# Kernel optimization log

Hardware: AMD Instinct MI355X
Metric: run time of the kernel (lower is better)

The kernel has to match this reference:

```python
import jax, jax.numpy as jnp
import numpy as np


def setup_inputs() -> dict:
    key = jax.random.key(0)
    k1, k2, k3, k4 = jax.random.split(key, 4)
    B, Tv, Ta, D = 8, 2048, 2048, 256
    return {
        "visual_features": jax.random.normal(k1, (B, Tv, D), dtype=jnp.float32),
        "audio_features": jax.random.normal(k2, (B, Ta, D), dtype=jnp.float32),
        "visual_weights": jax.random.uniform(k3, (D, D), dtype=jnp.float32),
        "audio_weights": jax.random.uniform(k4, (D, D), dtype=jnp.float32),
        "num_neighbors": 8,
    }


def _pairwise_l2(vm, am):
    # ||v - a|| via the expanded form to avoid the [B,Tv,Ta,D] intermediate.
    sq = (
        jnp.sum(vm * vm, -1)[:, :, None]
        + jnp.sum(am * am, -1)[:, None, :]
        - 2.0 * jnp.einsum("btd,bsd->bts", vm, am)
    )
    sq = jnp.maximum(sq, 0.0)
    # safe sqrt: subgradient 0 at 0 (matches torch.norm backward convention)
    return jnp.where(sq > 0, jnp.sqrt(jnp.where(sq > 0, sq, 1.0)), 0.0)


def reference(visual_features, audio_features, visual_weights, audio_weights, num_neighbors):
    vm = visual_features @ visual_weights  # [B,Tv,D]
    am = audio_features @ audio_weights    # [B,Ta,D]
    graph = jnp.exp(-_pairwise_l2(vm, am))  # [B,Tv,Ta]
    # topk over the visual axis (dim=1): move it last for lax.top_k
    _, idx = jax.lax.top_k(jnp.swapaxes(graph, 1, 2), num_neighbors)  # [B,Ta,k]
    idx = jnp.swapaxes(idx, 1, 2)  # [B,k,Ta]
    # broadcasted gather along axis 1: result [B,k,Ta,D]
    vn = jnp.take_along_axis(visual_features[:, :, None, :], idx[..., None], axis=1)
    an = jnp.take_along_axis(audio_features[:, :, None, :], idx[..., None], axis=1)
    # mean over dim=2 (the Ta axis of the gathered neighbors) -> [B,k,D]
    return vn.mean(axis=2), an.mean(axis=2)
```

## Files before the change

kernel.cpp:

```cpp
#include <hip/hip_runtime.h>
#include <cstddef>
#include <cstdint>

namespace {
constexpr int kB   = 8;
constexpr int kT   = 2048;
constexpr int kD   = 256;
constexpr int kK   = 8;
constexpr int kM   = kB * kT;
constexpr int kNC  = kB * kT;
constexpr int kColCap = 64;
constexpr int kOvCap  = 1 << 17;
constexpr int kStr = 264;
constexpr float kMinNormalF = 1.17549435e-38f;
}

typedef __attribute__((ext_vector_type(8)))  __bf16 bf16x8;
typedef __attribute__((ext_vector_type(16))) float  f32x16;

__device__ inline unsigned short f2bf_rne(float x) {
  unsigned u = __float_as_uint(x);
  unsigned r = (u + 0x7FFFu + ((u >> 16) & 1u)) >> 16;
  return (unsigned short)r;
}
__device__ inline float bf2f(unsigned short h) {
  return __uint_as_float((unsigned)h << 16);
}
union FragU { uint4 u4; bf16x8 v; };

__device__ inline void async16(const unsigned short* g, unsigned short* l) {
  __builtin_amdgcn_global_load_lds(
      (const __attribute__((address_space(1))) unsigned int*)(const void*)g,
      (__attribute__((address_space(3))) unsigned int*)(void*)l, 16, 0, 0);
}

__device__ inline void stage_tile_async(const unsigned short* src,
                                        unsigned short* S, int w, int lane) {
  const int hi = lane >> 5, lo = lane & 31;
#pragma unroll
  for (int i = 0; i < 8; ++i) {
    const int p = w * 8 + i;
    const int rowl = p * 2 + hi;
    const int c = lo ^ (rowl & 31);
    async16(src + (size_t)rowl * kD + c * 8, S + p * 512);
  }
}
__device__ inline uint4 lds_frag(const unsigned short* S, int row, int kc, int half) {
  const int c = (kc * 2 + half) ^ (row & 31);
  return *reinterpret_cast<const uint4*>(S + row * 256 + c * 8);
}

__global__ __launch_bounds__(256) void prep(const float* __restrict__ W0,
                                            const float* __restrict__ W1,
                                            unsigned short* __restrict__ T0,
                                            unsigned short* __restrict__ T1,
                                            unsigned* __restrict__ zeroBase,
                                            int zeroWords,
                                            unsigned* __restrict__ outW) {
  const int blk = blockIdx.x;
  if (blk < 128) {
    const float* W = (blk & 64) ? W1 : W0;
    unsigned short* WT = (blk & 64) ? T1 : T0;
    const int t = blk & 63;
    const int c0 = (t & 7) * 32, k0 = (t >> 3) * 32;
    __shared__ float tile[32][33];
    const int tx = threadIdx.x & 31, ty = threadIdx.x >> 5;
#pragma unroll
    for (int i = 0; i < 4; ++i)
      tile[ty + i * 8][tx] = W[(size_t)(k0 + ty + i * 8) * kD + c0 + tx];
    __syncthreads();
#pragma unroll
    for (int i = 0; i < 4; ++i)
      WT[(size_t)(c0 + ty + i * 8) * kD + k0 + tx] = f2bf_rne(tile[tx][ty + i * 8]);
  } else {
    for (int i = (blk - 128) * 256 + threadIdx.x; i < zeroWords; i += 32 * 256)
      zeroBase[i] = 0u;
    for (int i = (blk - 128) * 256 + threadIdx.x; i < 2 * kB * kK * kD; i += 32 * 256)
      outW[i] = 0u;
  }
}

__global__ __launch_bounds__(256) void gemm_hyb(const float* __restrict__ Xv,
                                                const float* __restrict__ Xa,
                                                const unsigned short* __restrict__ WvT,
                                                const unsigned short* __restrict__ WaT,
                                                unsigned short* __restrict__ Cv,
                                                unsigned short* __restrict__ Ca,
                                                float* __restrict__ nv,
                                                float* __restrict__ na) {
  __shared__ unsigned short S[64 * kStr + 64 * 256];
  unsigned short* bufA = S;
  unsigned short* bufB = S + 64 * kStr;
  const int z = blockIdx.z;
  const float* X = z ? Xa : Xv;
  const unsigned short* WT = z ? WaT : WvT;
  unsigned short* Cb = z ? Ca : Cv;
  float* nrm = z ? na : nv;
  const int r0 = blockIdx.x * 64;
  const int tid = threadIdx.x;
  const int w = tid >> 6, lane = tid & 63;
  const int wt = w & 1, wc = w >> 1;
  const int half = lane >> 5, ln = lane & 31;

#pragma unroll
  for (int i = 0; i < 16; ++i) {
    const int idx = i * 256 + tid;
    const int row = idx >> 6, g = idx & 63;
    const float4 v = *reinterpret_cast<const float4*>(X + (size_t)(r0 + row) * kD + g * 4);
    ushort4 o;
    o.x = f2bf_rne(v.x); o.y = f2bf_rne(v.y); o.z = f2bf_rne(v.z); o.w = f2bf_rne(v.w);
    *reinterpret_cast<ushort4*>(bufA + row * kStr + g * 4) = o;
  }
  __syncthreads();

  stage_tile_async(WT, bufB, w, lane);
  uint4 afr[16];
#pragma unroll
  for (int kc = 0; kc < 16; ++kc)
    afr[kc] = *reinterpret_cast<const uint4*>(bufA + (wt * 32 + ln) * kStr + kc * 16 + half * 8);
  __syncthreads();

  float ns[16];
#pragma unroll
  for (int r = 0; r < 16; ++r) ns[r] = 0.0f;

  for (int ct = 0; ct < 4; ++ct) {
    unsigned short* cur = (ct & 1) ? bufA : bufB;
    unsigned short* nxt = (ct & 1) ? bufB : bufA;
    if (ct < 3)
      stage_tile_async(WT + (size_t)(ct + 1) * 64 * kD, nxt, w, lane);
    const int c0 = ct * 64;
    f32x16 acc;
#pragma unroll
    for (int i = 0; i < 16; ++i) acc[i] = 0.0f;
#pragma unroll
    for (int kc = 0; kc < 16; ++kc) {
      FragU fa, fb;
      fa.u4 = afr[kc];
      fb.u4 = lds_frag(cur, wc * 32 + ln, kc, half);
      acc = __builtin_amdgcn_mfma_f32_32x32x16_bf16(fa.v, fb.v, acc, 0, 0, 0);
    }
    const int col = c0 + wc * 32 + ln;
#pragma unroll
    for (int r = 0; r < 16; ++r) {
      const int row = r0 + wt * 32 + (r & 3) + 8 * (r >> 2) + 4 * half;
      const unsigned short us = f2bf_rne(acc[r]);
      Cb[(size_t)row * kD + col] = us;
      const float f = bf2f(us);
      ns[r] += f * f;
    }
    if (ct < 3) __syncthreads();
  }
#pragma unroll
  for (int r = 0; r < 16; ++r) {
    float v = ns[r];
#pragma unroll
    for (int off = 1; off < 32; off <<= 1) v += __shfl_xor(v, off, 64);
    if (ln == 0) {
      const int row = r0 + wt * 32 + (r & 3) + 8 * (r >> 2) + 4 * half;
      atomicAdd(nrm + row, v);
    }
  }
}

__global__ __launch_bounds__(256, 4) void keys_v16(const unsigned short* __restrict__ vmb,
                                                   const unsigned short* __restrict__ amb,
                                                   const float* __restrict__ vn2,
                                                   const float* __restrict__ an2,
                                                   unsigned* __restrict__ colCount,
                                                   uint2* __restrict__ colRecs,
                                                   unsigned* __restrict__ ovCount,
                                                   uint2* __restrict__ ovRecs) {
  __shared__ unsigned short S[64 * 256];
  const int hw = blockIdx.x + (blockIdx.y << 4) + (blockIdx.z << 7);
  const int lg = ((hw & 7) << 7) | (hw >> 3);
  const int b = lg >> 7;
  const int t0 = (lg & 15) << 7;
  const int sr0 = ((lg >> 4) & 7) << 8;
  const int tid = threadIdx.x;
  const int w = tid >> 6, lane = tid & 63;
  const int half = lane >> 5, ln = lane & 31;

  uint4 afr[16];
#pragma unroll
  for (int h = 0; h < 2; ++h) {
    __syncthreads();
    stage_tile_async(vmb + ((size_t)b * kT + t0 + h * 64) * kD, S, w, lane);
    __syncthreads();
    if ((w >> 1) == h) {
#pragma unroll
      for (int kc = 0; kc < 16; ++kc)
        afr[kc] = lds_frag(S, (w & 1) * 32 + ln, kc, half);
    }
  }

  const float* v2p = vn2 + (size_t)b * kT + t0 + w * 32;

  for (int st = 0; st < 4; ++st) {
    const int s0 = sr0 + st * 64;
    __syncthreads();
    stage_tile_async(amb + ((size_t)b * kT + s0) * kD, S, w, lane);
    __syncthreads();
#pragma unroll
    for (int ss = 0; ss < 2; ++ss) {
      f32x16 acc;
#pragma unroll
      for (int i = 0; i < 16; ++i) acc[i] = 0.0f;
#pragma unroll
      for (int kc = 0; kc < 16; ++kc) {
        FragU fa, fb;
        fa.u4 = afr[kc];
        fb.u4 = lds_frag(S, ss * 32 + ln, kc, half);
        acc = __builtin_amdgcn_mfma_f32_32x32x16_bf16(fa.v, fb.v, acc, 0, 0, 0);
      }
      const int s = s0 + ss * 32 + ln;
      const float a2 = an2[(size_t)b * kT + s];
      const int c = (b << 11) | s;
#pragma unroll
      for (int g = 0; g < 4; ++g) {
        const float4 v2 = *reinterpret_cast<const float4*>(v2p + g * 8 + half * 4);
        const float v2a[4] = {v2.x, v2.y, v2.z, v2.w};
#pragma unroll
        for (int q = 0; q < 4; ++q) {
          const float raw = v2a[q] + a2 - 2.0f * acc[4 * g + q];
          if (raw < 7744.0f) {
            const float dist = sqrtf(fmaxf(raw, 0.0f));
            const float e = expf(-dist);
            if (e >= kMinNormalF) {
              const int t = t0 + w * 32 + g * 8 + half * 4 + q;
              const unsigned slot = atomicAdd(&colCount[c], 1u);
              if (slot < (unsigned)kColCap) {
                colRecs[(size_t)c * kColCap + slot] = make_uint2(__float_as_uint(e), (unsigned)t);
              } else {
                const unsigned pos = ((unsigned)b << 22) | ((unsigned)s << 11) | (unsigned)t;
                const unsigned oi = atomicAdd(ovCount, 1u);
                if (oi < (unsigned)kOvCap) ovRecs[oi] = make_uint2(__float_as_uint(e), pos);
              }
            }
          }
        }
      }
    }
  }
}

__global__ __launch_bounds__(256) void gather_fused(const float* __restrict__ visual,
                                                    const float* __restrict__ audio,
                                                    const unsigned* __restrict__ colCount,
                                                    const uint2* __restrict__ colRecs,
                                                    const unsigned* __restrict__ ovCount,
                                                    const uint2* __restrict__ ovRecs,
                                                    float* __restrict__ out) {
  __shared__ int sIdx[32];
  const int u = blockIdx.x;
  const int bj = u >> 6, ch = u & 63;
  const int b = bj >> 3, j = bj & 7;
  const int tid = threadIdx.x;
  if (tid < 32) {
    const int s = ch * 32 + tid;
    const int c = (b << 11) | s;
    unsigned K[8]; int T[8];
#pragma unroll
    for (int i = 0; i < 8; ++i) { K[i] = 0u; T[i] = 0x7FFFFFFF; }
    const int cnt = (int)colCount[c];
    const int m = min(cnt, kColCap);
    for (int i = 0; i < m; ++i) {
      const uint2 r = colRecs[(size_t)c * kColCap + i];
      const unsigned kx = r.x; const int tx = (int)r.y;
      if (kx > K[7] || (kx == K[7] && tx < T[7])) {
        K[7] = kx; T[7] = tx;
#pragma unroll
        for (int q = 7; q >= 1; --q) {
          const bool sw = (K[q] > K[q - 1]) || (K[q] == K[q - 1] && T[q] < T[q - 1]);
          if (sw) {
            const unsigned tk = K[q]; K[q] = K[q - 1]; K[q - 1] = tk;
            const int tt = T[q];      T[q] = T[q - 1]; T[q - 1] = tt;
          }
        }
      }
    }
    if (cnt > kColCap) {
      int n = (int)*ovCount;
      if (n > kOvCap) n = kOvCap;
      for (int i = 0; i < n; ++i) {
        const uint2 r = ovRecs[i];
        if ((int)(r.y >> 11) == c) {
          const unsigned kx = r.x; const int tx = (int)(r.y & 2047u);
          if (kx > K[7] || (kx == K[7] && tx < T[7])) {
            K[7] = kx; T[7] = tx;
#pragma unroll
            for (int q = 7; q >= 1; --q) {
              const bool sw = (K[q] > K[q - 1]) || (K[q] == K[q - 1] && T[q] < T[q - 1]);
              if (sw) {
                const unsigned tk = K[q]; K[q] = K[q - 1]; K[q - 1] = tk;
                const int tt = T[q];      T[q] = T[q - 1]; T[q - 1] = tt;
              }
            }
          }
        }
      }
    }
    int mcnt = 0;
#pragma unroll
    for (int i = 0; i < 8; ++i) if (K[i] > 0u) mcnt++;
    int outv[8];
#pragma unroll
    for (int i = 0; i < 8; ++i) outv[i] = T[i];
    int cand = 0;
    for (int r = mcnt; r < 8; ++r) {
      bool taken = true;
      while (taken) {
        taken = false;
#pragma unroll
        for (int q = 0; q < 8; ++q)
          if (q < mcnt && T[q] == cand) taken = true;
        if (taken) cand++;
      }
      outv[r] = cand++;
    }
    sIdx[tid] = outv[j];
  }
  __syncthreads();
  float accV = 0.f, accA = 0.f;
  for (int i = 0; i < 32; ++i) {
    const int t = sIdx[i];
    const size_t base = ((size_t)b * kT + t) * kD + tid;
    accV += visual[base];
    accA += audio[base];
  }
  atomicAdd(&out[(size_t)bj * kD + tid], accV * (1.0f / kT));
  atomicAdd(&out[(size_t)kB * kK * kD + (size_t)bj * kD + tid], accA * (1.0f / kT));
}

extern "C" void kernel_launch(void* const* d_in, const int* in_sizes, int n_in,
                              void* d_out, int out_size, void* d_ws, size_t ws_size,
                              hipStream_t stream) {
  (void)in_sizes; (void)n_in; (void)out_size; (void)ws_size;
  const float* visual = (const float*)d_in[0];
  const float* audio  = (const float*)d_in[1];
  const float* Wv     = (const float*)d_in[2];
  const float* Wa     = (const float*)d_in[3];
  float* out = (float*)d_out;

  char* ws = (char*)d_ws;
  unsigned short* WvT = (unsigned short*)ws;
  unsigned short* WaT = WvT + (size_t)kD * kD;
  unsigned short* vmb = WaT + (size_t)kD * kD;
  unsigned short* amb = vmb + (size_t)kM * kD;
  float* vn2 = (float*)(amb + (size_t)kM * kD);
  float* an2 = vn2 + kM;
  unsigned* colCount = (unsigned*)(an2 + kM);
  unsigned* ovCount  = colCount + kNC;
  uint2* colRecs = (uint2*)(ovCount + 8);
  uint2* ovRecs  = colRecs + (size_t)kNC * kColCap;
  const int zeroWords = 2 * kM + kNC + 8;

  prep<<<dim3(160), 256, 0, stream>>>(Wv, Wa, WvT, WaT, (unsigned*)vn2, zeroWords,
                                      (unsigned*)out);
  gemm_hyb<<<dim3(kM / 64, 1, 2), 256, 0, stream>>>(visual, audio, WvT, WaT,
                                                    vmb, amb, vn2, an2);
  keys_v16<<<dim3(kT / 128, kT / 256, kB), 256, 0, stream>>>(vmb, amb, vn2, an2,
                                                             colCount, colRecs, ovCount, ovRecs);
  gather_fused<<<dim3(4096), 256, 0, stream>>>(visual, audio, colCount, colRecs,
                                               ovCount, ovRecs, out);
}
```

Measured before the change: 176.1 us.

## Load MFMA fragments directly from global memory instead of staging through LDS

The distance/key kernel no longer stages visual and audio tiles through shared memory with block-wide barriers. Each lane loads its bf16 fragments straight from global memory (relying on L2/L1 reuse across waves), and the two 32-column sub-tiles are computed with two interleaved accumulators. The launch-bounds occupancy hint is dropped. This removes LDS traffic and __syncthreads stalls but issues redundant, less coalesced global loads across the four waves and uses more registers.

```diff
diff --git a/kernel.cpp b/kernel.cpp
--- a/kernel.cpp
+++ b/kernel.cpp
@@ -163,15 +163,14 @@
   }
 }
 
-__global__ __launch_bounds__(256, 4) void keys_v16(const unsigned short* __restrict__ vmb,
-                                                   const unsigned short* __restrict__ amb,
-                                                   const float* __restrict__ vn2,
-                                                   const float* __restrict__ an2,
-                                                   unsigned* __restrict__ colCount,
-                                                   uint2* __restrict__ colRecs,
-                                                   unsigned* __restrict__ ovCount,
-                                                   uint2* __restrict__ ovRecs) {
-  __shared__ unsigned short S[64 * 256];
+__global__ __launch_bounds__(256) void keys_v17(const unsigned short* __restrict__ vmb,
+                                                const unsigned short* __restrict__ amb,
+                                                const float* __restrict__ vn2,
+                                                const float* __restrict__ an2,
+                                                unsigned* __restrict__ colCount,
+                                                uint2* __restrict__ colRecs,
+                                                unsigned* __restrict__ ovCount,
+                                                uint2* __restrict__ ovRecs) {
   const int hw = blockIdx.x + (blockIdx.y << 4) + (blockIdx.z << 7);
   const int lg = ((hw & 7) << 7) | (hw >> 3);
   const int b = lg >> 7;
@@ -181,48 +180,49 @@
   const int w = tid >> 6, lane = tid & 63;
   const int half = lane >> 5, ln = lane & 31;
 
+  const uint4* vrow = reinterpret_cast<const uint4*>(
+      vmb + ((size_t)b * kT + t0 + w * 32 + ln) * kD);
   uint4 afr[16];
 #pragma unroll
-  for (int h = 0; h < 2; ++h) {
-    __syncthreads();
-    stage_tile_async(vmb + ((size_t)b * kT + t0 + h * 64) * kD, S, w, lane);
-    __syncthreads();
-    if ((w >> 1) == h) {
-#pragma unroll
-      for (int kc = 0; kc < 16; ++kc)
-        afr[kc] = lds_frag(S, (w & 1) * 32 + ln, kc, half);
-    }
-  }
+  for (int kc = 0; kc < 16; ++kc) afr[kc] = vrow[kc * 2 + half];
 
   const float* v2p = vn2 + (size_t)b * kT + t0 + w * 32;
 
   for (int st = 0; st < 4; ++st) {
     const int s0 = sr0 + st * 64;
-    __syncthreads();
-    stage_tile_async(amb + ((size_t)b * kT + s0) * kD, S, w, lane);
-    __syncthreads();
-#pragma unroll
-    for (int ss = 0; ss < 2; ++ss) {
-      f32x16 acc;
-#pragma unroll
-      for (int i = 0; i < 16; ++i) acc[i] = 0.0f;
-#pragma unroll
-      for (int kc = 0; kc < 16; ++kc) {
-        FragU fa, fb;
-        fa.u4 = afr[kc];
-        fb.u4 = lds_frag(S, ss * 32 + ln, kc, half);
-        acc = __builtin_amdgcn_mfma_f32_32x32x16_bf16(fa.v, fb.v, acc, 0, 0, 0);
-      }
-      const int s = s0 + ss * 32 + ln;
-      const float a2 = an2[(size_t)b * kT + s];
-      const int c = (b << 11) | s;
-#pragma unroll
-      for (int g = 0; g < 4; ++g) {
-        const float4 v2 = *reinterpret_cast<const float4*>(v2p + g * 8 + half * 4);
-        const float v2a[4] = {v2.x, v2.y, v2.z, v2.w};
+    const uint4* arow0 = reinterpret_cast<const uint4*>(
+        amb + ((size_t)b * kT + s0 + ln) * kD);
+    const uint4* arow1 = reinterpret_cast<const uint4*>(
+        amb + ((size_t)b * kT + s0 + 32 + ln) * kD);
+    f32x16 acc0, acc1;
+#pragma unroll
+    for (int i = 0; i < 16; ++i) { acc0[i] = 0.0f; acc1[i] = 0.0f; }
+#pragma unroll 4
+    for (int kc = 0; kc < 16; ++kc) {
+      FragU fa, f0, f1;
+      fa.u4 = afr[kc];
+      f0.u4 = arow0[kc * 2 + half];
+      f1.u4 = arow1[kc * 2 + half];
+      acc0 = __builtin_amdgcn_mfma_f32_32x32x16_bf16(fa.v, f0.v, acc0, 0, 0, 0);
+      acc1 = __builtin_amdgcn_mfma_f32_32x32x16_bf16(fa.v, f1.v, acc1, 0, 0, 0);
+    }
+    float a2s[2];
+#pragma unroll
+    for (int ss = 0; ss < 2; ++ss)
+      a2s[ss] = an2[(size_t)b * kT + s0 + ss * 32 + ln];
+#pragma unroll
+    for (int g = 0; g < 4; ++g) {
+      const float4 v2 = *reinterpret_cast<const float4*>(v2p + g * 8 + half * 4);
+      const float v2a[4] = {v2.x, v2.y, v2.z, v2.w};
+#pragma unroll
+      for (int ss = 0; ss < 2; ++ss) {
+        const int s = s0 + ss * 32 + ln;
+        const float a2 = a2s[ss];
+        const int c = (b << 11) | s;
 #pragma unroll
         for (int q = 0; q < 4; ++q) {
-          const float raw = v2a[q] + a2 - 2.0f * acc[4 * g + q];
+          const float av = ss ? acc1[4 * g + q] : acc0[4 * g + q];
+          const float raw = v2a[q] + a2 - 2.0f * av;
           if (raw < 7744.0f) {
             const float dist = sqrtf(fmaxf(raw, 0.0f));
             const float e = expf(-dist);
@@ -359,7 +359,7 @@
                                       (unsigned*)out);
   gemm_hyb<<<dim3(kM / 64, 1, 2), 256, 0, stream>>>(visual, audio, WvT, WaT,
                                                     vmb, amb, vn2, an2);
-  keys_v16<<<dim3(kT / 128, kT / 256, kB), 256, 0, stream>>>(vmb, amb, vn2, an2,
+  keys_v17<<<dim3(kT / 128, kT / 256, kB), 256, 0, stream>>>(vmb, amb, vn2, an2,
                                                              colCount, colRecs, ovCount, ovRecs);
   gather_fused<<<dim3(4096), 256, 0, stream>>>(visual, audio, colCount, colRecs,
                                                ovCount, ovRecs, out);
```

Result: slower. 248.1 us (+40.9%).
